# Performance work log

Hardware: AMD Instinct MI355X
Metric: run time of the kernel (lower is better)

The kernel has to match this reference:

```python
import jax, jax.numpy as jnp
import numpy as np

HIDDEN = 4096
NH = 32          # num attention heads
NKV = 8          # num key/value heads
HD = HIDDEN // NH  # 128
THETA = 10000.0
WINDOW = 4096    # sliding window hard-coded in forward


def _rotate_half(x):
    x1, x2 = jnp.split(x, 2, axis=-1)
    return jnp.concatenate((-x2, x1), axis=-1)


def setup_inputs() -> dict:
    key = jax.random.key(0)
    ks = jax.random.split(key, 5)
    B, S = 1, 2048
    hidden_states = jax.random.normal(ks[0], (B, S, HIDDEN), jnp.float32)
    position_ids = jnp.broadcast_to(jnp.arange(S, dtype=jnp.int64), (B, S))
    s = 0.02
    q_w = jax.random.normal(ks[1], (HIDDEN, NH * HD), jnp.float32) * s
    k_w = jax.random.normal(ks[2], (HIDDEN, NKV * HD), jnp.float32) * s
    v_w = jax.random.normal(ks[3], (HIDDEN, NKV * HD), jnp.float32) * s
    o_w = jax.random.normal(ks[4], (NH * HD, HIDDEN), jnp.float32) * s
    return {"hidden_states": hidden_states, "position_ids": position_ids,
            "q_w": q_w, "k_w": k_w, "v_w": v_w, "o_w": o_w}


def reference(hidden_states, position_ids, q_w, k_w, v_w, o_w):
    B, S, _ = hidden_states.shape
    # projections (bias=False), split heads -> [B, H, S, D]
    q = (hidden_states @ q_w).reshape(B, S, NH, HD).transpose(0, 2, 1, 3)
    k = (hidden_states @ k_w).reshape(B, S, NKV, HD).transpose(0, 2, 1, 3)
    v = (hidden_states @ v_w).reshape(B, S, NKV, HD).transpose(0, 2, 1, 3)

    # rotary embedding cache (MistralRotaryEmbedding)
    inv_freq = 1.0 / (THETA ** (jnp.arange(0, HD, 2, dtype=jnp.float32) / HD))
    t = jnp.arange(S, dtype=jnp.float32)
    freqs = t[:, None] * inv_freq[None, :]           # [S, HD/2]
    emb = jnp.concatenate((freqs, freqs), axis=-1)   # [S, HD]
    cos = jnp.cos(emb)[position_ids][:, None]        # [B, 1, S, HD]
    sin = jnp.sin(emb)[position_ids][:, None]
    q = q * cos + _rotate_half(q) * sin
    k = k * cos + _rotate_half(k) * sin

    # GQA repeat_kv: [B, NKV, S, D] -> [B, NH, S, D]
    rep = NH // NKV
    k = jnp.repeat(k, rep, axis=1)
    v = jnp.repeat(v, rep, axis=1)

    # scores + sliding-window causal mask
    scale = 1.0 / np.sqrt(HD).astype(np.float32)
    w = jnp.einsum("bhqd,bhkd->bhqk", q, k) * scale  # [B, NH, S, S]
    i = jnp.arange(S)[:, None]
    j = jnp.arange(S)[None, :]
    allowed = (j <= i) & ((i - j) < WINDOW)
    neg = jnp.finfo(jnp.float32).min
    w = w + jnp.where(allowed, 0.0, neg)[None, None]

    # fp32 softmax (upcast as in HF Mistral)
    w = jax.nn.softmax(w.astype(jnp.float32), axis=-1).astype(q.dtype)

    out = jnp.einsum("bhqk,bhkd->bhqd", w, v)        # [B, NH, S, D]
    out = out.transpose(0, 2, 1, 3).reshape(B, S, NH * HD)
    return out @ o_w                                  # [B, S, HIDDEN]
```

## Files before the change

kernel.cpp:

```cpp
#include <hip/hip_runtime.h>
#include <hip/hip_bf16.h>

#define S 2048
#define HID 4096
#define NH 32
#define NKV 8
#define HD 128
#define QKVN 6144

typedef __attribute__((ext_vector_type(8))) short bf16x8;
typedef __attribute__((ext_vector_type(4))) float f32x4;
typedef __attribute__((ext_vector_type(8))) unsigned short u16x8;
typedef __attribute__((ext_vector_type(4))) unsigned short u16x4;

#define GLOAD16(src, dst)                                                        \
  __builtin_amdgcn_global_load_lds(                                              \
      (const __attribute__((address_space(1))) unsigned int*)(src),              \
      (__attribute__((address_space(3))) unsigned int*)(dst), 16, 0, 0)

__device__ __forceinline__ unsigned short f2bf(float f) {
  union { float f; unsigned u; } c; c.f = f;
  unsigned u = c.u;
  return (unsigned short)((u + 0x7FFFu + ((u >> 16) & 1u)) >> 16);
}
__device__ __forceinline__ float bf2f(unsigned short h) {
  union { unsigned u; float f; } c; c.u = ((unsigned)h) << 16;
  return c.f;
}

__global__ void convert_kernel(const float* __restrict__ in,
                               unsigned short* __restrict__ out, int n4) {
  int i = blockIdx.x * blockDim.x + threadIdx.x;
  if (i < n4) {
    float4 v = ((const float4*)in)[i];
    ushort4 o;
    o.x = f2bf(v.x); o.y = f2bf(v.y); o.z = f2bf(v.z); o.w = f2bf(v.w);
    ((ushort4*)out)[i] = o;
  }
}

__global__ void transpose_convert(const float* __restrict__ in,
                                  unsigned short* __restrict__ out, int N) {
  __shared__ float tile[32][33];
  int tx = threadIdx.x, ty = threadIdx.y;
  int n0 = blockIdx.x * 32, k0 = blockIdx.y * 32;
#pragma unroll
  for (int i = 0; i < 32; i += 8)
    tile[ty + i][tx] = in[(size_t)(k0 + ty + i) * N + n0 + tx];
  __syncthreads();
#pragma unroll
  for (int i = 0; i < 32; i += 8)
    out[(size_t)(n0 + ty + i) * HID + k0 + tx] = f2bf(tile[tx][ty + i]);
}

__device__ __forceinline__ void storeC(unsigned short* C, size_t idx, float v) { C[idx] = f2bf(v); }
__device__ __forceinline__ void storeC(float* C, size_t idx, float v) { C[idx] = v; }

template <typename OutT>
__launch_bounds__(256, 2)
__global__ void gemm_bt(const unsigned short* __restrict__ A,
                        const unsigned short* __restrict__ Bt,
                        OutT* __restrict__ C, int K, int ldc) {
  __shared__ unsigned short As[2][2][128 * 32];
  __shared__ unsigned short Bs[2][2][128 * 32];
  const int tid = threadIdx.x, lane = tid & 63, w = tid >> 6;
  const int wr = w >> 1, wc = w & 1;
  const int m0 = blockIdx.y * 128, n0 = blockIdx.x * 128;
  const int lq = lane & 15, g = lane >> 4;
  const int swz8 = (g ^ (lq & 3) ^ ((lq >> 2) & 3)) << 3;

  f32x4 acc[4][4] = {};
  const int NT = K >> 6;

  auto STAGE_PAIR = [&](int bb, int ss, int kt) {
#pragma unroll
    for (int i = 0; i < 2; ++i) {
      int ci = tid + i * 256;
      int row = ci >> 2;
      int jl = (((ci & 3) ^ (row & 3) ^ ((row >> 2) & 3))) << 3;
      GLOAD16(A + (size_t)(m0 + row) * K + kt + ss * 32 + jl, &As[bb][ss][ci * 8]);
      GLOAD16(Bt + (size_t)(n0 + row) * K + kt + ss * 32 + jl, &Bs[bb][ss][ci * 8]);
    }
  };

  STAGE_PAIR(0, 0, 0);
  STAGE_PAIR(0, 1, 0);

  for (int t = 0; t < NT; ++t) {
    const int c = t & 1;
    const bool more = (t + 1) < NT;
    const int kt1 = (t + 1) << 6;
#pragma unroll
    for (int s = 0; s < 2; ++s) {
      if (s == 0 || more) asm volatile("s_waitcnt vmcnt(4)" ::: "memory");
      else                asm volatile("s_waitcnt vmcnt(0)" ::: "memory");
      __builtin_amdgcn_s_barrier();

      bf16x8 af[4], bfr[4];
#pragma unroll
      for (int mi = 0; mi < 4; ++mi)
        af[mi] = *(const bf16x8*)&As[c][s][(wr * 64 + mi * 16 + lq) * 32 + swz8];
#pragma unroll
      for (int ni = 0; ni < 4; ++ni)
        bfr[ni] = *(const bf16x8*)&Bs[c][s][(wc * 64 + ni * 16 + lq) * 32 + swz8];

      if (more) STAGE_PAIR(c ^ 1, s, kt1);

      asm volatile("s_waitcnt lgkmcnt(0)" ::: "memory");
      __builtin_amdgcn_sched_barrier(0);
      __builtin_amdgcn_s_setprio(1);
#pragma unroll
      for (int mi = 0; mi < 4; ++mi)
#pragma unroll
        for (int ni = 0; ni < 4; ++ni)
          acc[mi][ni] = __builtin_amdgcn_mfma_f32_16x16x32_bf16(af[mi], bfr[ni], acc[mi][ni], 0, 0, 0);
      __builtin_amdgcn_s_setprio(0);
    }
  }

#pragma unroll
  for (int mi = 0; mi < 4; ++mi) {
#pragma unroll
    for (int ni = 0; ni < 4; ++ni) {
      int row = m0 + wr * 64 + mi * 16 + g * 4;
      int col = n0 + wc * 64 + ni * 16 + lq;
#pragma unroll
      for (int r = 0; r < 4; ++r)
        storeC(C, (size_t)(row + r) * ldc + col, acc[mi][ni][r]);
    }
  }
}

template <typename OutT>
__launch_bounds__(512, 1)
__global__ void gemm256_bt(const unsigned short* __restrict__ A,
                           const unsigned short* __restrict__ Bt,
                           OutT* __restrict__ C, int K, int ldc) {
  __shared__ unsigned short As[2][256 * 64];
  __shared__ unsigned short Bs[2][256 * 64];
  const int tid = threadIdx.x, lane = tid & 63, w = tid >> 6;
  const int wm = w >> 2, wn = w & 3;
  const int m0 = blockIdx.y * 256, n0 = blockIdx.x * 256;
  const int lq = lane & 15, g = lane >> 4;
  const int sw = lq & 7;

  f32x4 acc[8][4] = {};
  const int NT = K >> 6;

  auto STAGE_PAIR = [&](int bb, int kt) {
#pragma unroll
    for (int i = 0; i < 4; ++i) {
      int ci = tid + i * 512;
      int r = ci >> 3;
      int jl = ((ci & 7) ^ (r & 7)) << 3;
      GLOAD16(A + (size_t)(m0 + r) * K + kt + jl, &As[bb][ci * 8]);
      GLOAD16(Bt + (size_t)(n0 + r) * K + kt + jl, &Bs[bb][ci * 8]);
    }
  };

  STAGE_PAIR(0, 0);

  for (int t = 0; t < NT; ++t) {
    const int c = t & 1;
    const bool more = (t + 1) < NT;

    asm volatile("s_waitcnt vmcnt(0)" ::: "memory");
    __builtin_amdgcn_s_barrier();
    bf16x8 af[8], bf[4];
#pragma unroll
    for (int mi = 0; mi < 8; ++mi)
      af[mi] = *(const bf16x8*)&As[c][(wm * 128 + mi * 16 + lq) * 64 + ((g ^ sw) << 3)];
#pragma unroll
    for (int ni = 0; ni < 4; ++ni)
      bf[ni] = *(const bf16x8*)&Bs[c][(wn * 64 + ni * 16 + lq) * 64 + ((g ^ sw) << 3)];
    if (more) STAGE_PAIR(c ^ 1, (t + 1) << 6);
    asm volatile("s_waitcnt lgkmcnt(0)" ::: "memory");
    __builtin_amdgcn_sched_barrier(0);
    __builtin_amdgcn_s_setprio(1);
#pragma unroll
    for (int mi = 0; mi < 8; ++mi)
#pragma unroll
      for (int ni = 0; ni < 4; ++ni)
        acc[mi][ni] = __builtin_amdgcn_mfma_f32_16x16x32_bf16(af[mi], bf[ni], acc[mi][ni], 0, 0, 0);
    __builtin_amdgcn_s_setprio(0);

#pragma unroll
    for (int mi = 0; mi < 8; ++mi)
      af[mi] = *(const bf16x8*)&As[c][(wm * 128 + mi * 16 + lq) * 64 + (((4 + g) ^ sw) << 3)];
#pragma unroll
    for (int ni = 0; ni < 4; ++ni)
      bf[ni] = *(const bf16x8*)&Bs[c][(wn * 64 + ni * 16 + lq) * 64 + (((4 + g) ^ sw) << 3)];
    asm volatile("s_waitcnt lgkmcnt(0)" ::: "memory");
    __builtin_amdgcn_sched_barrier(0);
    __builtin_amdgcn_s_setprio(1);
#pragma unroll
    for (int mi = 0; mi < 8; ++mi)
#pragma unroll
      for (int ni = 0; ni < 4; ++ni)
        acc[mi][ni] = __builtin_amdgcn_mfma_f32_16x16x32_bf16(af[mi], bf[ni], acc[mi][ni], 0, 0, 0);
    __builtin_amdgcn_s_setprio(0);
  }

#pragma unroll
  for (int mi = 0; mi < 8; ++mi)
#pragma unroll
    for (int ni = 0; ni < 4; ++ni) {
      int row = m0 + wm * 128 + mi * 16 + g * 4;
      int col = n0 + wn * 64 + ni * 16 + lq;
#pragma unroll
      for (int r = 0; r < 4; ++r)
        storeC(C, (size_t)(row + r) * ldc + col, acc[mi][ni][r]);
    }
}

__global__ void rope_kernel(unsigned short* __restrict__ qkv) {
  int idx = blockIdx.x * blockDim.x + threadIdx.x;
  int d = idx & 63;
  int h = (idx >> 6) % (NH + NKV);
  int s = (idx >> 6) / (NH + NKV);
  size_t base = (size_t)s * QKVN + (h < NH ? h * HD : NH * HD + (h - NH) * HD);
  float invf = __expf(-(float)d * (1.0f / 64.0f) * 9.210340371976184f);
  float ang = (float)s * invf;
  float c, sn;
  __sincosf(ang, &sn, &c);
  float x1 = bf2f(qkv[base + d]);
  float x2 = bf2f(qkv[base + d + 64]);
  float o1 = x1 * c - x2 * sn;
  float o2 = x2 * c + x1 * sn;
  if (h < NH) {
    o1 *= 0.08838834764831845f;
    o2 *= 0.08838834764831845f;
  }
  qkv[base + d] = f2bf(o1);
  qkv[base + d + 64] = f2bf(o2);
}

__launch_bounds__(512, 4)
__global__ void attn_kernel(const unsigned short* __restrict__ qkv,
                            unsigned short* __restrict__ ao) {
  __shared__ unsigned short Ks[2][64 * 128];
  __shared__ unsigned short Vt[128 * 88];
  __shared__ unsigned short Ps[8][16 * 88];

  const int tid = threadIdx.x, lane = tid & 63, w = tid >> 6;
  const int b = blockIdx.x;
  const int h = blockIdx.y;
  const int qblk = (h < 16) ? (15 - b) : b;
  const int kh = h >> 2;
  const int lq = lane & 15, g = lane >> 4;
  const int qbase = qblk * 128 + w * 16;
  const size_t koff = (size_t)NH * HD + (size_t)kh * HD;
  const size_t voff = (size_t)(NH + NKV) * HD + (size_t)kh * HD;

  bf16x8 qf[4];
  {
    const unsigned short* qp = qkv + (size_t)(qbase + lq) * QKVN + (size_t)h * HD + g * 8;
#pragma unroll
    for (int ks = 0; ks < 4; ++ks) qf[ks] = *(const bf16x8*)(qp + ks * 32);
  }

  f32x4 o[8] = {};
  float m = -1e30f;
  float l = 0.f;

  auto KSTAGE = [&](int bb, int kv0) {
#pragma unroll
    for (int i = 0; i < 2; ++i) {
      int kvk = (w * 2 + i) * 4 + (lane >> 4);
      int chl = (lane & 15) ^ (kvk & 7);
      GLOAD16(qkv + (size_t)(kv0 + kvk) * QKVN + koff + chl * 8, &Ks[bb][(w * 2 + i) * 512]);
    }
  };
  const int vd0 = (tid & 31) * 4;
  const int vkv = (tid >> 5) * 4;
  u16x4 vr[4];
  auto VLOAD = [&](int kv0) {
#pragma unroll
    for (int i = 0; i < 4; ++i)
      vr[i] = *(const u16x4*)(qkv + (size_t)(kv0 + vkv + i) * QKVN + voff + vd0);
  };
  auto VWRITE = [&]() {
#pragma unroll
    for (int j = 0; j < 4; ++j) {
      const int d = vd0 + j;
      const int vswz = ((d >> 3) & 3) << 1;
      const int vcol = (((vkv >> 2) ^ vswz) << 2);
      u16x4 val = {vr[0][j], vr[1][j], vr[2][j], vr[3][j]};
      *(u16x4*)&Vt[d * 88 + vcol] = val;
    }
  };

  unsigned short* Pw = &Ps[w][0];
  const int nt = qblk * 2 + 2;

  KSTAGE(0, 0);
  VLOAD(0);
  int cur = 0;
  for (int t = 0; t < nt; ++t) {
    const int kv0 = t * 64;
    __syncthreads();
    VWRITE();
    __syncthreads();
    if (t + 1 < nt) { KSTAGE(cur ^ 1, kv0 + 64); VLOAD(kv0 + 64); }

    const int nraw = qbase + 16 - kv0;
    const int nact = nraw > 64 ? 64 : nraw;

    f32x4 sc[4];
    __builtin_amdgcn_s_setprio(1);
#pragma unroll
    for (int st = 0; st < 4; ++st) {
      if (st * 16 < nact) {
        f32x4 s = {};
#pragma unroll
        for (int ks = 0; ks < 4; ++ks) {
          const bf16x8 kf = *(const bf16x8*)
              &Ks[cur][(st * 16 + lq) * 128 + (((ks * 4 + g) ^ (lq & 7)) << 3)];
          s = __builtin_amdgcn_mfma_f32_16x16x32_bf16(kf, qf[ks], s, 0, 0, 0);
        }
        sc[st] = s;
      } else {
        sc[st] = (f32x4){-1e30f, -1e30f, -1e30f, -1e30f};
      }
    }
    __builtin_amdgcn_s_setprio(0);
    if (nraw < 79) {
      const int q = qbase + lq;
#pragma unroll
      for (int st = 0; st < 4; ++st) {
        int kv = kv0 + st * 16 + g * 4;
#pragma unroll
        for (int r = 0; r < 4; ++r)
          if (kv + r > q) sc[st][r] = -1e30f;
      }
    }

    float mn = fmaxf(fmaxf(fmaxf(sc[0][0], sc[0][1]), fmaxf(sc[0][2], sc[0][3])),
                     fmaxf(fmaxf(sc[1][0], sc[1][1]), fmaxf(sc[1][2], sc[1][3])));
    mn = fmaxf(mn, fmaxf(fmaxf(fmaxf(sc[2][0], sc[2][1]), fmaxf(sc[2][2], sc[2][3])),
                         fmaxf(fmaxf(sc[3][0], sc[3][1]), fmaxf(sc[3][2], sc[3][3]))));
    mn = fmaxf(mn, __shfl_xor(mn, 16, 64));
    mn = fmaxf(mn, __shfl_xor(mn, 32, 64));
    const bool need = __any(mn > m);
    const float m2 = fmaxf(m, mn);
    const float alpha = __expf(m - m2);
    m = m2;
    float rs = 0.f;
#pragma unroll
    for (int st = 0; st < 4; ++st)
#pragma unroll
      for (int r = 0; r < 4; ++r) {
        float p = __expf(sc[st][r] - m2);
        sc[st][r] = p;
        rs += p;
      }
    rs += __shfl_xor(rs, 16, 64);
    rs += __shfl_xor(rs, 32, 64);
    l = l * alpha + rs;

    if (need) {
      float alphaR[4];
#pragma unroll
      for (int r = 0; r < 4; ++r) alphaR[r] = __shfl(alpha, g * 4 + r, 64);
#pragma unroll
      for (int p = 0; p < 8; ++p)
#pragma unroll
        for (int r = 0; r < 4; ++r) o[p][r] *= alphaR[r];
    }

#pragma unroll
    for (int st = 0; st < 4; ++st) {
      unsigned r01, r23;
      asm("v_cvt_pk_bf16_f32 %0, %1, %2" : "=v"(r01) : "v"(sc[st][0]), "v"(sc[st][1]));
      asm("v_cvt_pk_bf16_f32 %0, %1, %2" : "=v"(r23) : "v"(sc[st][2]), "v"(sc[st][3]));
      unsigned* dst = (unsigned*)&Pw[lq * 88 + st * 16 + g * 4];
      dst[0] = r01; dst[1] = r23;
    }

    const int nks = nact > 0 ? (nact + 31) >> 5 : 0;
    __builtin_amdgcn_s_setprio(1);
    for (int ks = 0; ks < nks; ++ks) {
      const bf16x8 pf = *(const bf16x8*)&Pw[lq * 88 + ks * 32 + g * 8];
#pragma unroll
      for (int p = 0; p < 8; ++p) {
        const int d = p * 16 + lq;
        const int rswz = ((d >> 3) & 3) << 1;
        const int kvc = (ks * 8 + g * 2) ^ rswz;
        const bf16x8 vf = *(const bf16x8*)&Vt[d * 88 + (kvc << 2)];
        o[p] = __builtin_amdgcn_mfma_f32_16x16x32_bf16(pf, vf, o[p], 0, 0, 0);
      }
    }
    __builtin_amdgcn_s_setprio(0);

    cur ^= 1;
  }

  float invR[4];
#pragma unroll
  for (int r = 0; r < 4; ++r) invR[r] = 1.0f / __shfl(l, g * 4 + r, 64);
#pragma unroll
  for (int p = 0; p < 8; ++p)
#pragma unroll
    for (int r = 0; r < 4; ++r)
      ao[(size_t)(qbase + g * 4 + r) * (NH * HD) + (size_t)h * HD + p * 16 + lq] =
          f2bf(o[p][r] * invR[r]);
}

extern "C" void kernel_launch(void* const* d_in, const int* in_sizes, int n_in,
                              void* d_out, int out_size, void* d_ws, size_t ws_size,
                              hipStream_t stream) {
  const float* X  = (const float*)d_in[0];
  const float* qw = (const float*)d_in[2];
  const float* kw = (const float*)d_in[3];
  const float* vw = (const float*)d_in[4];
  const float* ow = (const float*)d_in[5];
  float* out = (float*)d_out;

  char* ws = (char*)d_ws;
  unsigned short* Xb  = (unsigned short*)(ws);
  unsigned short* Wt  = (unsigned short*)(ws + (size_t)(16u << 20));
  unsigned short* QKV = (unsigned short*)(ws + (size_t)(64u << 20));
  unsigned short* AO  = (unsigned short*)(ws + (size_t)(88u << 20));
  unsigned short* OWt = (unsigned short*)(ws);

  dim3 tb(32, 8);

  convert_kernel<<<(S * HID / 4 + 255) / 256, 256, 0, stream>>>(X, Xb, S * HID / 4);
  transpose_convert<<<dim3(HID / 32, HID / 32), tb, 0, stream>>>(qw, Wt, HID);
  transpose_convert<<<dim3((NKV * HD) / 32, HID / 32), tb, 0, stream>>>(kw, Wt + (size_t)(NH * HD) * HID, NKV * HD);
  transpose_convert<<<dim3((NKV * HD) / 32, HID / 32), tb, 0, stream>>>(vw, Wt + (size_t)(NH + NKV) * HD * HID, NKV * HD);
  gemm256_bt<unsigned short><<<dim3(QKVN / 256, S / 256), 512, 0, stream>>>(Xb, Wt, QKV, HID, QKVN);
  transpose_convert<<<dim3(HID / 32, HID / 32), tb, 0, stream>>>(ow, OWt, HID);
  rope_kernel<<<(S * (NH + NKV) * 64) / 256, 256, 0, stream>>>(QKV);
  attn_kernel<<<dim3(16, NH), 512, 0, stream>>>(QKV, AO);
  gemm_bt<float><<<dim3(HID / 128, S / 128), 256, 0, stream>>>(AO, OWt, out, HID, HID);
}
```

Baseline: 319.9 us.

## Pre-transpose V globally and load PV fragments straight from global memory

```diff
diff --git a/kernel.cpp b/kernel.cpp
--- a/kernel.cpp
+++ b/kernel.cpp
@@ -51,6 +51,20 @@
 #pragma unroll
   for (int i = 0; i < 32; i += 8)
     out[(size_t)(n0 + ty + i) * HID + k0 + tx] = f2bf(tile[tx][ty + i]);
+}
+
+__global__ void transpose_v(const unsigned short* __restrict__ qkv,
+                            unsigned short* __restrict__ vtg) {
+  __shared__ unsigned short tile[32][33];
+  int tx = threadIdx.x, ty = threadIdx.y;
+  int s0 = blockIdx.x * 32, d0 = blockIdx.y * 32;
+#pragma unroll
+  for (int i = 0; i < 32; i += 8)
+    tile[ty + i][tx] = qkv[(size_t)(s0 + ty + i) * QKVN + (NH + NKV) * HD + d0 + tx];
+  __syncthreads();
+#pragma unroll
+  for (int i = 0; i < 32; i += 8)
+    vtg[(size_t)(d0 + ty + i) * S + s0 + tx] = tile[tx][ty + i];
 }
 
 __device__ __forceinline__ void storeC(unsigned short* C, size_t idx, float v) { C[idx] = f2bf(v); }
@@ -237,9 +251,9 @@
 
 __launch_bounds__(512, 4)
 __global__ void attn_kernel(const unsigned short* __restrict__ qkv,
+                            const unsigned short* __restrict__ vtg,
                             unsigned short* __restrict__ ao) {
   __shared__ unsigned short Ks[2][64 * 128];
-  __shared__ unsigned short Vt[128 * 88];
   __shared__ unsigned short Ps[8][16 * 88];
 
   const int tid = threadIdx.x, lane = tid & 63, w = tid >> 6;
@@ -250,7 +264,6 @@
   const int lq = lane & 15, g = lane >> 4;
   const int qbase = qblk * 128 + w * 16;
   const size_t koff = (size_t)NH * HD + (size_t)kh * HD;
-  const size_t voff = (size_t)(NH + NKV) * HD + (size_t)kh * HD;
 
   bf16x8 qf[4];
   {
@@ -271,37 +284,24 @@
       GLOAD16(qkv + (size_t)(kv0 + kvk) * QKVN + koff + chl * 8, &Ks[bb][(w * 2 + i) * 512]);
     }
   };
-  const int vd0 = (tid & 31) * 4;
-  const int vkv = (tid >> 5) * 4;
-  u16x4 vr[4];
-  auto VLOAD = [&](int kv0) {
-#pragma unroll
-    for (int i = 0; i < 4; ++i)
-      vr[i] = *(const u16x4*)(qkv + (size_t)(kv0 + vkv + i) * QKVN + voff + vd0);
-  };
-  auto VWRITE = [&]() {
-#pragma unroll
-    for (int j = 0; j < 4; ++j) {
-      const int d = vd0 + j;
-      const int vswz = ((d >> 3) & 3) << 1;
-      const int vcol = (((vkv >> 2) ^ vswz) << 2);
-      u16x4 val = {vr[0][j], vr[1][j], vr[2][j], vr[3][j]};
-      *(u16x4*)&Vt[d * 88 + vcol] = val;
-    }
-  };
+
+  const unsigned short* vbase = vtg + ((size_t)kh * 128 + lq) * S + g * 8;
 
   unsigned short* Pw = &Ps[w][0];
   const int nt = qblk * 2 + 2;
 
   KSTAGE(0, 0);
-  VLOAD(0);
   int cur = 0;
   for (int t = 0; t < nt; ++t) {
     const int kv0 = t * 64;
     __syncthreads();
-    VWRITE();
-    __syncthreads();
-    if (t + 1 < nt) { KSTAGE(cur ^ 1, kv0 + 64); VLOAD(kv0 + 64); }
+
+    bf16x8 vf0[8];
+#pragma unroll
+    for (int p = 0; p < 8; ++p)
+      vf0[p] = *(const bf16x8*)(vbase + (size_t)p * 16 * S + kv0);
+    __builtin_amdgcn_sched_barrier(0);
+    if (t + 1 < nt) KSTAGE(cur ^ 1, kv0 + 64);
 
     const int nraw = qbase + 16 - kv0;
     const int nact = nraw > 64 ? 64 : nraw;
@@ -378,19 +378,28 @@
     }
 
     const int nks = nact > 0 ? (nact + 31) >> 5 : 0;
-    __builtin_amdgcn_s_setprio(1);
-    for (int ks = 0; ks < nks; ++ks) {
-      const bf16x8 pf = *(const bf16x8*)&Pw[lq * 88 + ks * 32 + g * 8];
-#pragma unroll
-      for (int p = 0; p < 8; ++p) {
-        const int d = p * 16 + lq;
-        const int rswz = ((d >> 3) & 3) << 1;
-        const int kvc = (ks * 8 + g * 2) ^ rswz;
-        const bf16x8 vf = *(const bf16x8*)&Vt[d * 88 + (kvc << 2)];
-        o[p] = __builtin_amdgcn_mfma_f32_16x16x32_bf16(pf, vf, o[p], 0, 0, 0);
-      }
-    }
-    __builtin_amdgcn_s_setprio(0);
+    if (nks > 0) {
+      bf16x8 vf1[8];
+      if (nks > 1) {
+#pragma unroll
+        for (int p = 0; p < 8; ++p)
+          vf1[p] = *(const bf16x8*)(vbase + (size_t)p * 16 * S + kv0 + 32);
+      }
+      __builtin_amdgcn_s_setprio(1);
+      {
+        const bf16x8 pf = *(const bf16x8*)&Pw[lq * 88 + g * 8];
+#pragma unroll
+        for (int p = 0; p < 8; ++p)
+          o[p] = __builtin_amdgcn_mfma_f32_16x16x32_bf16(pf, vf0[p], o[p], 0, 0, 0);
+      }
+      if (nks > 1) {
+        const bf16x8 pf = *(const bf16x8*)&Pw[lq * 88 + 32 + g * 8];
+#pragma unroll
+        for (int p = 0; p < 8; ++p)
+          o[p] = __builtin_amdgcn_mfma_f32_16x16x32_bf16(pf, vf1[p], o[p], 0, 0, 0);
+      }
+      __builtin_amdgcn_s_setprio(0);
+    }
 
     cur ^= 1;
   }
@@ -422,6 +431,7 @@
   unsigned short* QKV = (unsigned short*)(ws + (size_t)(64u << 20));
   unsigned short* AO  = (unsigned short*)(ws + (size_t)(88u << 20));
   unsigned short* OWt = (unsigned short*)(ws);
+  unsigned short* Vtg = (unsigned short*)(ws + (size_t)(32u << 20));
 
   dim3 tb(32, 8);
 
@@ -432,6 +442,7 @@
   gemm256_bt<unsigned short><<<dim3(QKVN / 256, S / 256), 512, 0, stream>>>(Xb, Wt, QKV, HID, QKVN);
   transpose_convert<<<dim3(HID / 32, HID / 32), tb, 0, stream>>>(ow, OWt, HID);
   rope_kernel<<<(S * (NH + NKV) * 64) / 256, 256, 0, stream>>>(QKV);
-  attn_kernel<<<dim3(16, NH), 512, 0, stream>>>(QKV, AO);
+  transpose_v<<<dim3(S / 32, (NKV * HD) / 32), tb, 0, stream>>>(QKV, Vtg);
+  attn_kernel<<<dim3(16, NH), 512, 0, stream>>>(QKV, Vtg, AO);
   gemm_bt<float><<<dim3(HID / 128, S / 128), 256, 0, stream>>>(AO, OWt, out, HID, HID);
 }
```

Measured after the change: 554.8 us. +73.5%, slower.

## Restructure gemm_bt LDS staging into single 64-wide K tile per stage

Applied to the files above, without the earlier changes.

```diff
diff --git a/kernel.cpp b/kernel.cpp
--- a/kernel.cpp
+++ b/kernel.cpp
@@ -61,61 +61,69 @@
 __global__ void gemm_bt(const unsigned short* __restrict__ A,
                         const unsigned short* __restrict__ Bt,
                         OutT* __restrict__ C, int K, int ldc) {
-  __shared__ unsigned short As[2][2][128 * 32];
-  __shared__ unsigned short Bs[2][2][128 * 32];
+  __shared__ unsigned short As[2][128 * 64];
+  __shared__ unsigned short Bs[2][128 * 64];
   const int tid = threadIdx.x, lane = tid & 63, w = tid >> 6;
   const int wr = w >> 1, wc = w & 1;
   const int m0 = blockIdx.y * 128, n0 = blockIdx.x * 128;
   const int lq = lane & 15, g = lane >> 4;
-  const int swz8 = (g ^ (lq & 3) ^ ((lq >> 2) & 3)) << 3;
+  const int sw = lq & 7;
 
   f32x4 acc[4][4] = {};
   const int NT = K >> 6;
 
-  auto STAGE_PAIR = [&](int bb, int ss, int kt) {
-#pragma unroll
-    for (int i = 0; i < 2; ++i) {
+  auto STAGE_PAIR = [&](int bb, int kt) {
+#pragma unroll
+    for (int i = 0; i < 4; ++i) {
       int ci = tid + i * 256;
-      int row = ci >> 2;
-      int jl = (((ci & 3) ^ (row & 3) ^ ((row >> 2) & 3))) << 3;
-      GLOAD16(A + (size_t)(m0 + row) * K + kt + ss * 32 + jl, &As[bb][ss][ci * 8]);
-      GLOAD16(Bt + (size_t)(n0 + row) * K + kt + ss * 32 + jl, &Bs[bb][ss][ci * 8]);
+      int r = ci >> 3;
+      int jl = ((ci & 7) ^ (r & 7)) << 3;
+      GLOAD16(A + (size_t)(m0 + r) * K + kt + jl, &As[bb][ci * 8]);
+      GLOAD16(Bt + (size_t)(n0 + r) * K + kt + jl, &Bs[bb][ci * 8]);
     }
   };
 
-  STAGE_PAIR(0, 0, 0);
-  STAGE_PAIR(0, 1, 0);
+  STAGE_PAIR(0, 0);
 
   for (int t = 0; t < NT; ++t) {
     const int c = t & 1;
     const bool more = (t + 1) < NT;
-    const int kt1 = (t + 1) << 6;
-#pragma unroll
-    for (int s = 0; s < 2; ++s) {
-      if (s == 0 || more) asm volatile("s_waitcnt vmcnt(4)" ::: "memory");
-      else                asm volatile("s_waitcnt vmcnt(0)" ::: "memory");
-      __builtin_amdgcn_s_barrier();
-
-      bf16x8 af[4], bfr[4];
-#pragma unroll
-      for (int mi = 0; mi < 4; ++mi)
-        af[mi] = *(const bf16x8*)&As[c][s][(wr * 64 + mi * 16 + lq) * 32 + swz8];
+
+    asm volatile("s_waitcnt vmcnt(0)" ::: "memory");
+    __builtin_amdgcn_s_barrier();
+    bf16x8 af[4], bf[4];
+#pragma unroll
+    for (int mi = 0; mi < 4; ++mi)
+      af[mi] = *(const bf16x8*)&As[c][(wr * 64 + mi * 16 + lq) * 64 + ((g ^ sw) << 3)];
+#pragma unroll
+    for (int ni = 0; ni < 4; ++ni)
+      bf[ni] = *(const bf16x8*)&Bs[c][(wc * 64 + ni * 16 + lq) * 64 + ((g ^ sw) << 3)];
+    if (more) STAGE_PAIR(c ^ 1, (t + 1) << 6);
+    asm volatile("s_waitcnt lgkmcnt(0)" ::: "memory");
+    __builtin_amdgcn_sched_barrier(0);
+    __builtin_amdgcn_s_setprio(1);
+#pragma unroll
+    for (int mi = 0; mi < 4; ++mi)
 #pragma unroll
       for (int ni = 0; ni < 4; ++ni)
-        bfr[ni] = *(const bf16x8*)&Bs[c][s][(wc * 64 + ni * 16 + lq) * 32 + swz8];
-
-      if (more) STAGE_PAIR(c ^ 1, s, kt1);
-
-      asm volatile("s_waitcnt lgkmcnt(0)" ::: "memory");
-      __builtin_amdgcn_sched_barrier(0);
-      __builtin_amdgcn_s_setprio(1);
-#pragma unroll
-      for (int mi = 0; mi < 4; ++mi)
-#pragma unroll
-        for (int ni = 0; ni < 4; ++ni)
-          acc[mi][ni] = __builtin_amdgcn_mfma_f32_16x16x32_bf16(af[mi], bfr[ni], acc[mi][ni], 0, 0, 0);
-      __builtin_amdgcn_s_setprio(0);
-    }
+        acc[mi][ni] = __builtin_amdgcn_mfma_f32_16x16x32_bf16(af[mi], bf[ni], acc[mi][ni], 0, 0, 0);
+    __builtin_amdgcn_s_setprio(0);
+
+#pragma unroll
+    for (int mi = 0; mi < 4; ++mi)
+      af[mi] = *(const bf16x8*)&As[c][(wr * 64 + mi * 16 + lq) * 64 + (((4 + g) ^ sw) << 3)];
+#pragma unroll
+    for (int ni = 0; ni < 4; ++ni)
+      bf[ni] = *(const bf16x8*)&Bs[c][(wc * 64 + ni * 16 + lq) * 64 + (((4 + g) ^ sw) << 3)];
+    asm volatile("s_waitcnt lgkmcnt(0)" ::: "memory");
+    __builtin_amdgcn_sched_barrier(0);
+    __builtin_amdgcn_s_setprio(1);
+#pragma unroll
+    for (int mi = 0; mi < 4; ++mi)
+#pragma unroll
+      for (int ni = 0; ni < 4; ++ni)
+        acc[mi][ni] = __builtin_amdgcn_mfma_f32_16x16x32_bf16(af[mi], bf[ni], acc[mi][ni], 0, 0, 0);
+    __builtin_amdgcn_s_setprio(0);
   }
 
 #pragma unroll
```

After: 311.2 us. 2.7% less time.
